# Performance work log

Hardware: AMD Instinct MI355X
Metric: run time of the kernel (lower is better)

## Reference

```python
import jax, jax.numpy as jnp
import numpy as np

DIM = 512
H = 8
HD = DIM // H  # head_dim = 64


def setup_inputs() -> dict:
    key = jax.random.key(0)
    k1, k2, k3 = jax.random.split(key, 3)
    B, N = 16, 4096
    x = jax.random.normal(k1, (B, DIM, N), jnp.float32)
    # qkv_proj: Conv1d(dim, H*(1+2*HD), kernel=1) == linear over channels
    Wqkv = jax.random.normal(k2, (H * (1 + 2 * HD), DIM), jnp.float32) * 0.02
    bqkv = jnp.zeros((H * (1 + 2 * HD),), jnp.float32)
    # proj: Conv1d(dim, dim, kernel=1)
    Wp = jax.random.normal(k3, (DIM, DIM), jnp.float32) * 0.02
    bp = jnp.zeros((DIM,), jnp.float32)
    return {"x": x, "Wqkv": Wqkv, "bqkv": bqkv, "Wp": Wp, "bp": bp}


def reference(x, Wqkv, bqkv, Wp, bp):
    B, C, N = x.shape
    # 1x1 conv projection -> [B, H*(1+2*HD), N]
    qkv = jnp.einsum('oc,bcn->bon', Wqkv, x) + bqkv[None, :, None]
    qkv = qkv.reshape(B, H, 1 + 2 * HD, N)
    q = qkv[:, :, 0:1, :]          # [B,H,1,N]
    k = qkv[:, :, 1:1 + HD, :]     # [B,H,HD,N]
    v = qkv[:, :, 1 + HD:, :]      # [B,H,HD,N]
    scores = jax.nn.softmax(q, axis=-1)              # softmax over N
    ctx = jnp.sum(k * scores, axis=-1, keepdims=True)  # [B,H,HD,1]
    out = jax.nn.relu(v) * ctx                         # [B,H,HD,N]
    # permute/split/cat in torch == [B,H,HD,N] -> [B,N,H*HD] -> [B,C,N]
    out = out.transpose(0, 3, 1, 2).reshape(B, N, H * HD)
    out = out.transpose(0, 2, 1)                       # [B,C,N]
    out = jnp.einsum('oc,bcn->bon', Wp, out) + bp[None, :, None]
    return out
```

## Files before the change

### kernel.cpp

```cpp
#include <hip/hip_runtime.h>

#define NB 16
#define NC 512
#define NN 4096
#define NH 8

typedef __attribute__((ext_vector_type(8))) __bf16 bf16x8;
typedef __attribute__((ext_vector_type(4))) float f32x4;

__device__ __forceinline__ unsigned short f2bf(float f) {
    union { float f; unsigned u; } x; x.f = f;
    unsigned r = x.u + 0x7FFF + ((x.u >> 16) & 1);
    return (unsigned short)(r >> 16);
}
__device__ __forceinline__ float bits2f(unsigned u) {
    union { unsigned u; float f; } x; x.u = u; return x.f;
}

__device__ __forceinline__ void async16(const void* g, const void* l) {
    __builtin_amdgcn_global_load_lds(
        (const __attribute__((address_space(1))) void*)g,
        (__attribute__((address_space(3))) void*)l, 16, 0, 0);
}

__global__ void pack_kernel(const float* __restrict__ Wqkv, const float* __restrict__ bqkv,
                            const float* __restrict__ Wp,
                            unsigned short* __restrict__ Wv_bf, unsigned short* __restrict__ Wp_bf,
                            float* __restrict__ bv) {
    int t = blockIdx.x * 256 + threadIdx.x;
    int j = t >> 9, c = t & 511;
    int h = j >> 6, d = j & 63;
    Wv_bf[t] = f2bf(Wqkv[((size_t)h * 129 + 65 + d) * 512 + c]);
    Wp_bf[t] = f2bf(Wp[t]);
    if (t < 512) bv[t] = bqkv[(t >> 6) * 129 + 65 + (t & 63)];
}

__global__ __launch_bounds__(256) void q_xbf_kernel(
        const float* __restrict__ x, const float* __restrict__ Wqkv,
        unsigned int* __restrict__ xbf, float* __restrict__ qP) {
    __shared__ float Ws[8][64];
    int n0 = blockIdx.x * 512, c0 = blockIdx.y * 64, b = blockIdx.z;
    int t = threadIdx.x;
    for (int i = t; i < 512; i += 256)
        Ws[i >> 6][i & 63] = Wqkv[(size_t)(i >> 6) * (129 * 512) + c0 + (i & 63)];
    __syncthreads();

    float acc[8][2];
#pragma unroll
    for (int h = 0; h < 8; h++) { acc[h][0] = 0.f; acc[h][1] = 0.f; }

    const float* xb = x + ((size_t)b * NC + c0) * NN + n0;
    unsigned int* ob = xbf + (((size_t)b * NC + c0) * NN + n0) / 2 + t;

#pragma unroll 4
    for (int c = 0; c < 64; c++) {
        float2 v = *((const float2*)(xb + (size_t)c * NN) + t);
        ob[(size_t)c * (NN / 2)] = (unsigned)f2bf(v.x) | ((unsigned)f2bf(v.y) << 16);
#pragma unroll
        for (int h = 0; h < 8; h++) {
            float w = Ws[h][c];
            acc[h][0] += w * v.x;
            acc[h][1] += w * v.y;
        }
    }
#pragma unroll
    for (int h = 0; h < 8; h++) {
        float2 o; o.x = acc[h][0]; o.y = acc[h][1];
        *((float2*)(qP + ((size_t)(blockIdx.y * NB + b) * 8 + h) * NN + n0) + t) = o;
    }
}

__global__ void softmax_kernel(const float* __restrict__ qP, float* __restrict__ sT) {
    int bh = blockIdx.x;
    int b = bh >> 3, h = bh & 7;
    int t = threadIdx.x;
    __shared__ float red[8];
    const float* qp = qP + (size_t)bh * NN;
    const size_t cstr = (size_t)NB * 8 * NN;
    float v[16];
    float mx = -1e30f;
#pragma unroll
    for (int i = 0; i < 16; i++) {
        int n = t + i * 256;
        float s = 0.f;
#pragma unroll
        for (int cb = 0; cb < 8; cb++) s += qp[cb * cstr + n];
        v[i] = s; mx = fmaxf(mx, s);
    }
#pragma unroll
    for (int o = 32; o; o >>= 1) mx = fmaxf(mx, __shfl_xor(mx, o));
    if ((t & 63) == 0) red[t >> 6] = mx;
    __syncthreads();
    mx = fmaxf(fmaxf(red[0], red[1]), fmaxf(red[2], red[3]));
    float s = 0.f;
#pragma unroll
    for (int i = 0; i < 16; i++) { v[i] = __expf(v[i] - mx); s += v[i]; }
#pragma unroll
    for (int o = 32; o; o >>= 1) s += __shfl_xor(s, o);
    __syncthreads();
    if ((t & 63) == 0) red[4 + (t >> 6)] = s;
    __syncthreads();
    float inv = 1.f / (red[4] + red[5] + red[6] + red[7]);
#pragma unroll
    for (int i = 0; i < 16; i++) {
        int n = t + i * 256;
        sT[((size_t)b * NN + n) * 8 + h] = v[i] * inv;
    }
}

__global__ __launch_bounds__(256) void xbar_kernel(
        const unsigned int* __restrict__ xbf, const float* __restrict__ sT,
        float* __restrict__ xbarP) {
    __shared__ float red[4][8][64];
    int c0 = blockIdx.x * 32, sl = blockIdx.y, b = blockIdx.z;
    int t = threadIdx.x;
    int l = t & 63, w = t >> 6;
    int nsl0 = sl * 512;
    float s_[8][8];
    {
        const f32x4* sp = (const f32x4*)(sT + ((size_t)b * NN + nsl0 + l * 8) * 8);
#pragma unroll
        for (int j = 0; j < 8; j++) {
            f32x4 a = sp[2 * j], bq = sp[2 * j + 1];
            s_[j][0] = a[0]; s_[j][1] = a[1]; s_[j][2] = a[2]; s_[j][3] = a[3];
            s_[j][4] = bq[0]; s_[j][5] = bq[1]; s_[j][6] = bq[2]; s_[j][7] = bq[3];
        }
    }
    float acc[8][8];
#pragma unroll
    for (int r = 0; r < 8; r++)
#pragma unroll
        for (int h = 0; h < 8; h++) acc[r][h] = 0.f;

    const unsigned int* xr = xbf + (((size_t)b * NC + c0 + w * 8) * NN + nsl0) / 2 + l * 4;
    uint4 xv = *(const uint4*)(xr);
#pragma unroll
    for (int r = 0; r < 8; r++) {
        uint4 cur = xv;
        if (r < 7) xv = *(const uint4*)(xr + (size_t)(r + 1) * (NN / 2));
        float xf[8];
        xf[0] = bits2f(cur.x << 16); xf[1] = bits2f(cur.x & 0xFFFF0000u);
        xf[2] = bits2f(cur.y << 16); xf[3] = bits2f(cur.y & 0xFFFF0000u);
        xf[4] = bits2f(cur.z << 16); xf[5] = bits2f(cur.z & 0xFFFF0000u);
        xf[6] = bits2f(cur.w << 16); xf[7] = bits2f(cur.w & 0xFFFF0000u);
#pragma unroll
        for (int j = 0; j < 8; j++)
#pragma unroll
            for (int h = 0; h < 8; h++) acc[r][h] += xf[j] * s_[j][h];
    }
#pragma unroll
    for (int r = 0; r < 8; r++)
#pragma unroll
        for (int h = 0; h < 8; h++) {
            float a = acc[r][h];
            a += __shfl_xor(a, 8);
            a += __shfl_xor(a, 16);
            a += __shfl_xor(a, 32);
            acc[r][h] = a;
        }
    if (l < 8) {
#pragma unroll
        for (int r = 0; r < 8; r++)
#pragma unroll
            for (int h = 0; h < 8; h++) red[w][l][r * 8 + h] = acc[r][h];
    }
    __syncthreads();
    {
        int idx = t & 63;
        float v = 0.f;
#pragma unroll
        for (int res = 0; res < 8; res++) v += red[w][res][idx];
        int r = idx >> 3, h = idx & 7;
        xbarP[(((size_t)sl * NB + b) * 8 + h) * NC + c0 + w * 8 + r] = v;
    }
}

__global__ void ctx_kernel(const float* __restrict__ xbarP, const float* __restrict__ Wqkv,
                           const float* __restrict__ bqkv, float* __restrict__ ctx) {
    int bh = blockIdx.x; int b = bh >> 3, h = bh & 7;
    int t = threadIdx.x;
    __shared__ float xb[512];
    for (int i = t; i < 512; i += 256) {
        float s = 0.f;
#pragma unroll
        for (int sl = 0; sl < 8; sl++) s += xbarP[(((size_t)sl * NB + b) * 8 + h) * NC + i];
        xb[i] = s;
    }
    __syncthreads();
    int d = t >> 2, sub = t & 3;
    const float* wk = Wqkv + ((size_t)h * 129 + 1 + d) * 512;
    float acc = 0.f;
    for (int i = sub * 4; i < 512; i += 16) {
        float4 w = *(const float4*)(wk + i);
        acc += w.x * xb[i] + w.y * xb[i + 1] + w.z * xb[i + 2] + w.w * xb[i + 3];
    }
    acc += __shfl_xor(acc, 1);
    acc += __shfl_xor(acc, 2);
    if (sub == 0) ctx[(size_t)b * NC + h * 64 + d] = acc + bqkv[h * 129 + 1 + d];
}

template <int MODE>
__global__ __launch_bounds__(512) void gemm_kernel(
    const unsigned short* __restrict__ A,
    const unsigned short* __restrict__ Bmat,
    const float* __restrict__ bias,
    const float* __restrict__ ctx,
    unsigned short* __restrict__ mT,
    float* __restrict__ outp)
{
    __shared__ alignas(16) unsigned short As[256 * 32];
    __shared__ alignas(16) unsigned short Bs[128 * 32];
    int b = blockIdx.z;
    int m0 = blockIdx.y * 256, n0 = blockIdx.x * 128;
    int t = threadIdx.x;
    int lane = t & 63;
    int wid = t >> 6;
    int wm = wid >> 1, wn = wid & 1;

    const unsigned short* Bb = Bmat + ((size_t)b * NN + n0) * NC;
    const unsigned int*   Bu = (const unsigned int*)Bmat + (size_t)b * NC * (NN / 2);

    int srow = lane >> 2, sc8 = (lane & 3) * 8;

    f32x4 acc[4][4];
#pragma unroll
    for (int i = 0; i < 4; i++)
#pragma unroll
        for (int j = 0; j < 4; j++) { f32x4 z = {0.f, 0.f, 0.f, 0.f}; acc[i][j] = z; }

    for (int kk = 0; kk < 512; kk += 32) {
        async16(A + (size_t)(m0 + wid * 32 + srow) * 512 + kk + sc8,      As + wid * 1024);
        async16(A + (size_t)(m0 + wid * 32 + 16 + srow) * 512 + kk + sc8, As + wid * 1024 + 512);
        if constexpr (MODE == 0) {
            int c = t >> 4, nb = (t & 15) * 8;
            uint4 xv = *(const uint4*)(Bu + ((size_t)(kk + c) * NN + n0 + nb) / 2);
            const unsigned short* xp16 = (const unsigned short*)&xv;
#pragma unroll
            for (int i = 0; i < 8; i++) {
                int nl = nb + i;
                int byte = nl * 64 + ((c * 2) ^ (((nl >> 3) & 3) << 4));
                *(unsigned short*)((char*)Bs + byte) = xp16[i];
            }
        } else {
            async16(Bb + (size_t)(wid * 16 + srow) * 512 + kk + sc8, Bs + wid * 512);
        }
        __syncthreads();
        bf16x8 af[4], bfr[4];
        int koff = (lane >> 4) * 8;
        int arow = wm * 64 + (lane & 15);
        int brow = wn * 64 + (lane & 15);
#pragma unroll
        for (int i = 0; i < 4; i++) af[i]  = *(const bf16x8*)(As + (size_t)(arow + i * 16) * 32 + koff);
#pragma unroll
        for (int j = 0; j < 4; j++) {
            if constexpr (MODE == 0) {
                int row = brow + j * 16;
                int byte = row * 64 + ((koff * 2) ^ (((row >> 3) & 3) << 4));
                bfr[j] = *(const bf16x8*)((const char*)Bs + byte);
            } else {
                bfr[j] = *(const bf16x8*)(Bs + (size_t)(brow + j * 16) * 32 + koff);
            }
        }
#pragma unroll
        for (int i = 0; i < 4; i++)
#pragma unroll
            for (int j = 0; j < 4; j++)
                acc[i][j] = __builtin_amdgcn_mfma_f32_16x16x32_bf16(af[i], bfr[j], acc[i][j], 0, 0, 0);
        __syncthreads();
    }

    int g = lane >> 4, col = lane & 15;
#pragma unroll
    for (int i = 0; i < 4; i++) {
        int j0 = m0 + wm * 64 + i * 16 + g * 4;
        if (MODE == 0) {
            float4 bv4 = *(const float4*)(bias + j0);
            float4 cx4 = *(const float4*)(ctx + (size_t)b * NC + j0);
#pragma unroll
            for (int j = 0; j < 4; j++) {
                int n = n0 + wn * 64 + j * 16 + col;
                f32x4 a = acc[i][j];
                unsigned short h0 = f2bf(fmaxf(a[0] + bv4.x, 0.f) * cx4.x);
                unsigned short h1 = f2bf(fmaxf(a[1] + bv4.y, 0.f) * cx4.y);
                unsigned short h2 = f2bf(fmaxf(a[2] + bv4.z, 0.f) * cx4.z);
                unsigned short h3 = f2bf(fmaxf(a[3] + bv4.w, 0.f) * cx4.w);
                uint2 pk;
                pk.x = (unsigned)h0 | ((unsigned)h1 << 16);
                pk.y = (unsigned)h2 | ((unsigned)h3 << 16);
                *(uint2*)(mT + ((size_t)b * NN + n) * NC + j0) = pk;
            }
        } else {
            float4 bp4 = *(const float4*)(bias + j0);
#pragma unroll
            for (int j = 0; j < 4; j++) {
                int n = n0 + wn * 64 + j * 16 + col;
                f32x4 a = acc[i][j];
                float* op = outp + (size_t)b * NC * NN + (size_t)j0 * NN + n;
                op[0]              = a[0] + bp4.x;
                op[NN]             = a[1] + bp4.y;
                op[2 * (size_t)NN] = a[2] + bp4.z;
                op[3 * (size_t)NN] = a[3] + bp4.w;
            }
        }
    }
}

extern "C" void kernel_launch(void* const* d_in, const int* in_sizes, int n_in,
                              void* d_out, int out_size, void* d_ws, size_t ws_size,
                              hipStream_t stream) {
    const float* x    = (const float*)d_in[0];
    const float* Wqkv = (const float*)d_in[1];
    const float* bqkv = (const float*)d_in[2];
    const float* Wp   = (const float*)d_in[3];
    const float* bp   = (const float*)d_in[4];
    float* outp = (float*)d_out;

    char* ws = (char*)d_ws;
    unsigned short* mT = (unsigned short*)ws;
    float* sT    = (float*)(ws + 2097152);
    float* qP    = (float*)(ws + 4194304);
    float* xbarP = (float*)(ws + 20971520);
    float* ctx   = (float*)(ws + 67108864);
    unsigned short* Wv_bf = (unsigned short*)(ws + 67108864 + 32768);
    unsigned short* Wp_bf = (unsigned short*)(ws + 67108864 + 32768 + 524288);
    float* bv    = (float*)(ws + 67108864 + 32768 + 1048576);
    unsigned int* xbf = (unsigned int*)d_out;

    pack_kernel<<<dim3(1024), 256, 0, stream>>>(Wqkv, bqkv, Wp, Wv_bf, Wp_bf, bv);
    q_xbf_kernel<<<dim3(8, 8, 16), 256, 0, stream>>>(x, Wqkv, xbf, qP);
    softmax_kernel<<<dim3(128), 256, 0, stream>>>(qP, sT);
    xbar_kernel<<<dim3(16, 8, 16), 256, 0, stream>>>(xbf, sT, xbarP);
    ctx_kernel<<<dim3(128), 256, 0, stream>>>(xbarP, Wqkv, bqkv, ctx);
    gemm_kernel<0><<<dim3(32, 2, 16), 512, 0, stream>>>(
        Wv_bf, (const unsigned short*)xbf, bv, ctx, mT, nullptr);
    gemm_kernel<1><<<dim3(32, 2, 16), 512, 0, stream>>>(
        Wp_bf, mT, bp, nullptr, nullptr, outp);
}
```

Before: 219.3 us.

## Fuse V-projection and output projection GEMMs, keeping intermediate in LDS

Merges the two GEMM kernels into one. Each block computes the full 512-channel V projection for a 128-column tile, applies relu and ctx scaling, stores the bf16 result in LDS, then runs the output projection from LDS. This removes the global round trip of the intermediate mT. The bf16 copy of x is dropped, so the q, xbar and fused kernels read fp32 x directly and convert on the fly. The cost is 144 KB of LDS per block, which limits occupancy, plus heavier register use and weights streamed straight from global memory into registers.

```diff
diff --git a/kernel.cpp b/kernel.cpp
--- a/kernel.cpp
+++ b/kernel.cpp
@@ -12,15 +12,6 @@
     union { float f; unsigned u; } x; x.f = f;
     unsigned r = x.u + 0x7FFF + ((x.u >> 16) & 1);
     return (unsigned short)(r >> 16);
-}
-__device__ __forceinline__ float bits2f(unsigned u) {
-    union { unsigned u; float f; } x; x.u = u; return x.f;
-}
-
-__device__ __forceinline__ void async16(const void* g, const void* l) {
-    __builtin_amdgcn_global_load_lds(
-        (const __attribute__((address_space(1))) void*)g,
-        (__attribute__((address_space(3))) void*)l, 16, 0, 0);
 }
 
 __global__ void pack_kernel(const float* __restrict__ Wqkv, const float* __restrict__ bqkv,
@@ -35,9 +26,9 @@
     if (t < 512) bv[t] = bqkv[(t >> 6) * 129 + 65 + (t & 63)];
 }
 
-__global__ __launch_bounds__(256) void q_xbf_kernel(
+__global__ __launch_bounds__(256) void q_kernel(
         const float* __restrict__ x, const float* __restrict__ Wqkv,
-        unsigned int* __restrict__ xbf, float* __restrict__ qP) {
+        float* __restrict__ qP) {
     __shared__ float Ws[8][64];
     int n0 = blockIdx.x * 512, c0 = blockIdx.y * 64, b = blockIdx.z;
     int t = threadIdx.x;
@@ -50,12 +41,9 @@
     for (int h = 0; h < 8; h++) { acc[h][0] = 0.f; acc[h][1] = 0.f; }
 
     const float* xb = x + ((size_t)b * NC + c0) * NN + n0;
-    unsigned int* ob = xbf + (((size_t)b * NC + c0) * NN + n0) / 2 + t;
-
 #pragma unroll 4
     for (int c = 0; c < 64; c++) {
         float2 v = *((const float2*)(xb + (size_t)c * NN) + t);
-        ob[(size_t)c * (NN / 2)] = (unsigned)f2bf(v.x) | ((unsigned)f2bf(v.y) << 16);
 #pragma unroll
         for (int h = 0; h < 8; h++) {
             float w = Ws[h][c];
@@ -109,7 +97,7 @@
 }
 
 __global__ __launch_bounds__(256) void xbar_kernel(
-        const unsigned int* __restrict__ xbf, const float* __restrict__ sT,
+        const float* __restrict__ x, const float* __restrict__ sT,
         float* __restrict__ xbarP) {
     __shared__ float red[4][8][64];
     int c0 = blockIdx.x * 32, sl = blockIdx.y, b = blockIdx.z;
@@ -132,17 +120,12 @@
 #pragma unroll
         for (int h = 0; h < 8; h++) acc[r][h] = 0.f;
 
-    const unsigned int* xr = xbf + (((size_t)b * NC + c0 + w * 8) * NN + nsl0) / 2 + l * 4;
-    uint4 xv = *(const uint4*)(xr);
+    const float* xr = x + ((size_t)b * NC + c0 + w * 8) * NN + nsl0 + l * 8;
 #pragma unroll
     for (int r = 0; r < 8; r++) {
-        uint4 cur = xv;
-        if (r < 7) xv = *(const uint4*)(xr + (size_t)(r + 1) * (NN / 2));
-        float xf[8];
-        xf[0] = bits2f(cur.x << 16); xf[1] = bits2f(cur.x & 0xFFFF0000u);
-        xf[2] = bits2f(cur.y << 16); xf[3] = bits2f(cur.y & 0xFFFF0000u);
-        xf[4] = bits2f(cur.z << 16); xf[5] = bits2f(cur.z & 0xFFFF0000u);
-        xf[6] = bits2f(cur.w << 16); xf[7] = bits2f(cur.w & 0xFFFF0000u);
+        float4 a0 = *(const float4*)(xr + (size_t)r * NN);
+        float4 a1 = *(const float4*)(xr + (size_t)r * NN + 4);
+        float xf[8] = {a0.x, a0.y, a0.z, a0.w, a1.x, a1.y, a1.z, a1.w};
 #pragma unroll
         for (int j = 0; j < 8; j++)
 #pragma unroll
@@ -199,108 +182,139 @@
     if (sub == 0) ctx[(size_t)b * NC + h * 64 + d] = acc + bqkv[h * 129 + 1 + d];
 }
 
-template <int MODE>
-__global__ __launch_bounds__(512) void gemm_kernel(
-    const unsigned short* __restrict__ A,
-    const unsigned short* __restrict__ Bmat,
-    const float* __restrict__ bias,
+__global__ __launch_bounds__(512, 2) void fused_gemm_kernel(
+    const unsigned short* __restrict__ Wv,
+    const unsigned short* __restrict__ Wp,
+    const float* __restrict__ x,
+    const float* __restrict__ bv,
+    const float* __restrict__ bp,
     const float* __restrict__ ctx,
-    unsigned short* __restrict__ mT,
     float* __restrict__ outp)
 {
-    __shared__ alignas(16) unsigned short As[256 * 32];
+    __shared__ alignas(16) unsigned short Ms[16 * 128 * 32];
     __shared__ alignas(16) unsigned short Bs[128 * 32];
-    int b = blockIdx.z;
-    int m0 = blockIdx.y * 256, n0 = blockIdx.x * 128;
-    int t = threadIdx.x;
-    int lane = t & 63;
-    int wid = t >> 6;
-    int wm = wid >> 1, wn = wid & 1;
-
-    const unsigned short* Bb = Bmat + ((size_t)b * NN + n0) * NC;
-    const unsigned int*   Bu = (const unsigned int*)Bmat + (size_t)b * NC * (NN / 2);
-
-    int srow = lane >> 2, sc8 = (lane & 3) * 8;
-
-    f32x4 acc[4][4];
-#pragma unroll
-    for (int i = 0; i < 4; i++)
+    int b = blockIdx.y, n0 = blockIdx.x * 128;
+    int t = threadIdx.x;
+    int lane = t & 63, wid = t >> 6;
+    int wj = wid >> 1, wn = wid & 1;
+    int g = lane >> 4, col = lane & 15;
+    int koff = g * 8;
+
+    int sc = t >> 4, sn8 = (t & 15) * 8;
+
+    f32x4 acc[8][4];
+#pragma unroll
+    for (int i = 0; i < 8; i++)
 #pragma unroll
         for (int j = 0; j < 4; j++) { f32x4 z = {0.f, 0.f, 0.f, 0.f}; acc[i][j] = z; }
 
-    for (int kk = 0; kk < 512; kk += 32) {
-        async16(A + (size_t)(m0 + wid * 32 + srow) * 512 + kk + sc8,      As + wid * 1024);
-        async16(A + (size_t)(m0 + wid * 32 + 16 + srow) * 512 + kk + sc8, As + wid * 1024 + 512);
-        if constexpr (MODE == 0) {
-            int c = t >> 4, nb = (t & 15) * 8;
-            uint4 xv = *(const uint4*)(Bu + ((size_t)(kk + c) * NN + n0 + nb) / 2);
-            const unsigned short* xp16 = (const unsigned short*)&xv;
+    bf16x8 afc[8], afn[8];
+#pragma unroll
+    for (int i = 0; i < 8; i++)
+        afc[i] = *(const bf16x8*)(Wv + (size_t)(wj * 128 + i * 16 + col) * 512 + koff);
+
+#pragma unroll 2
+    for (int ks = 0; ks < 16; ks++) {
+        int kk = ks * 32;
+        {
+            const float* xr = x + ((size_t)b * NC + kk + sc) * NN + n0 + sn8;
+            float4 v0 = *(const float4*)(xr);
+            float4 v1 = *(const float4*)(xr + 4);
+            unsigned short xv[8] = {f2bf(v0.x), f2bf(v0.y), f2bf(v0.z), f2bf(v0.w),
+                                    f2bf(v1.x), f2bf(v1.y), f2bf(v1.z), f2bf(v1.w)};
 #pragma unroll
             for (int i = 0; i < 8; i++) {
-                int nl = nb + i;
-                int byte = nl * 64 + ((c * 2) ^ (((nl >> 3) & 3) << 4));
-                *(unsigned short*)((char*)Bs + byte) = xp16[i];
+                int nl = sn8 + i;
+                int byte = nl * 64 + ((sc * 2) ^ (((nl >> 3) & 3) << 4));
+                *(unsigned short*)((char*)Bs + byte) = xv[i];
             }
-        } else {
-            async16(Bb + (size_t)(wid * 16 + srow) * 512 + kk + sc8, Bs + wid * 512);
+        }
+        if (ks < 15) {
+#pragma unroll
+            for (int i = 0; i < 8; i++)
+                afn[i] = *(const bf16x8*)(Wv + (size_t)(wj * 128 + i * 16 + col) * 512 + kk + 32 + koff);
         }
         __syncthreads();
-        bf16x8 af[4], bfr[4];
-        int koff = (lane >> 4) * 8;
-        int arow = wm * 64 + (lane & 15);
-        int brow = wn * 64 + (lane & 15);
-#pragma unroll
-        for (int i = 0; i < 4; i++) af[i]  = *(const bf16x8*)(As + (size_t)(arow + i * 16) * 32 + koff);
+        bf16x8 bfr[4];
 #pragma unroll
         for (int j = 0; j < 4; j++) {
-            if constexpr (MODE == 0) {
-                int row = brow + j * 16;
-                int byte = row * 64 + ((koff * 2) ^ (((row >> 3) & 3) << 4));
-                bfr[j] = *(const bf16x8*)((const char*)Bs + byte);
-            } else {
-                bfr[j] = *(const bf16x8*)(Bs + (size_t)(brow + j * 16) * 32 + koff);
-            }
-        }
-#pragma unroll
-        for (int i = 0; i < 4; i++)
+            int row = wn * 64 + j * 16 + col;
+            int byte = row * 64 + ((koff * 2) ^ (((row >> 3) & 3) << 4));
+            bfr[j] = *(const bf16x8*)((const char*)Bs + byte);
+        }
+#pragma unroll
+        for (int i = 0; i < 8; i++)
 #pragma unroll
             for (int j = 0; j < 4; j++)
-                acc[i][j] = __builtin_amdgcn_mfma_f32_16x16x32_bf16(af[i], bfr[j], acc[i][j], 0, 0, 0);
+                acc[i][j] = __builtin_amdgcn_mfma_f32_16x16x32_bf16(afc[i], bfr[j], acc[i][j], 0, 0, 0);
         __syncthreads();
-    }
-
-    int g = lane >> 4, col = lane & 15;
-#pragma unroll
-    for (int i = 0; i < 4; i++) {
-        int j0 = m0 + wm * 64 + i * 16 + g * 4;
-        if (MODE == 0) {
-            float4 bv4 = *(const float4*)(bias + j0);
-            float4 cx4 = *(const float4*)(ctx + (size_t)b * NC + j0);
-#pragma unroll
-            for (int j = 0; j < 4; j++) {
-                int n = n0 + wn * 64 + j * 16 + col;
-                f32x4 a = acc[i][j];
-                unsigned short h0 = f2bf(fmaxf(a[0] + bv4.x, 0.f) * cx4.x);
-                unsigned short h1 = f2bf(fmaxf(a[1] + bv4.y, 0.f) * cx4.y);
-                unsigned short h2 = f2bf(fmaxf(a[2] + bv4.z, 0.f) * cx4.z);
-                unsigned short h3 = f2bf(fmaxf(a[3] + bv4.w, 0.f) * cx4.w);
-                uint2 pk;
-                pk.x = (unsigned)h0 | ((unsigned)h1 << 16);
-                pk.y = (unsigned)h2 | ((unsigned)h3 << 16);
-                *(uint2*)(mT + ((size_t)b * NN + n) * NC + j0) = pk;
-            }
-        } else {
-            float4 bp4 = *(const float4*)(bias + j0);
-#pragma unroll
-            for (int j = 0; j < 4; j++) {
-                int n = n0 + wn * 64 + j * 16 + col;
-                f32x4 a = acc[i][j];
-                float* op = outp + (size_t)b * NC * NN + (size_t)j0 * NN + n;
-                op[0]              = a[0] + bp4.x;
-                op[NN]             = a[1] + bp4.y;
-                op[2 * (size_t)NN] = a[2] + bp4.z;
-                op[3 * (size_t)NN] = a[3] + bp4.w;
-            }
+#pragma unroll
+        for (int i = 0; i < 8; i++) afc[i] = afn[i];
+    }
+
+#pragma unroll
+    for (int i = 0; i < 8; i++) {
+        int j0 = wj * 128 + i * 16 + g * 4;
+        float4 bv4 = *(const float4*)(bv + j0);
+        float4 cx4 = *(const float4*)(ctx + (size_t)b * NC + j0);
+#pragma unroll
+        for (int j = 0; j < 4; j++) {
+            int n = wn * 64 + j * 16 + col;
+            f32x4 a = acc[i][j];
+            unsigned short h0 = f2bf(fmaxf(a[0] + bv4.x, 0.f) * cx4.x);
+            unsigned short h1 = f2bf(fmaxf(a[1] + bv4.y, 0.f) * cx4.y);
+            unsigned short h2 = f2bf(fmaxf(a[2] + bv4.z, 0.f) * cx4.z);
+            unsigned short h3 = f2bf(fmaxf(a[3] + bv4.w, 0.f) * cx4.w);
+            uint2 pk;
+            pk.x = (unsigned)h0 | ((unsigned)h1 << 16);
+            pk.y = (unsigned)h2 | ((unsigned)h3 << 16);
+            *(uint2*)(Ms + (size_t)(j0 >> 5) * 4096 + n * 32 + (j0 & 31)) = pk;
+        }
+    }
+    __syncthreads();
+
+#pragma unroll
+    for (int i = 0; i < 8; i++)
+#pragma unroll
+        for (int j = 0; j < 4; j++) { f32x4 z = {0.f, 0.f, 0.f, 0.f}; acc[i][j] = z; }
+#pragma unroll
+    for (int i = 0; i < 8; i++)
+        afc[i] = *(const bf16x8*)(Wp + (size_t)(wj * 128 + i * 16 + col) * 512 + koff);
+
+#pragma unroll 2
+    for (int ks = 0; ks < 16; ks++) {
+        int kk = ks * 32;
+        if (ks < 15) {
+#pragma unroll
+            for (int i = 0; i < 8; i++)
+                afn[i] = *(const bf16x8*)(Wp + (size_t)(wj * 128 + i * 16 + col) * 512 + kk + 32 + koff);
+        }
+        bf16x8 bfr[4];
+#pragma unroll
+        for (int j = 0; j < 4; j++)
+            bfr[j] = *(const bf16x8*)(Ms + (size_t)ks * 4096 + (wn * 64 + j * 16 + col) * 32 + koff);
+#pragma unroll
+        for (int i = 0; i < 8; i++)
+#pragma unroll
+            for (int j = 0; j < 4; j++)
+                acc[i][j] = __builtin_amdgcn_mfma_f32_16x16x32_bf16(afc[i], bfr[j], acc[i][j], 0, 0, 0);
+#pragma unroll
+        for (int i = 0; i < 8; i++) afc[i] = afn[i];
+    }
+
+#pragma unroll
+    for (int i = 0; i < 8; i++) {
+        int o0 = wj * 128 + i * 16 + g * 4;
+        float4 bp4 = *(const float4*)(bp + o0);
+#pragma unroll
+        for (int j = 0; j < 4; j++) {
+            int n = n0 + wn * 64 + j * 16 + col;
+            f32x4 a = acc[i][j];
+            float* op = outp + ((size_t)b * NC + o0) * NN + n;
+            op[0]              = a[0] + bp4.x;
+            op[NN]             = a[1] + bp4.y;
+            op[2 * (size_t)NN] = a[2] + bp4.z;
+            op[3 * (size_t)NN] = a[3] + bp4.w;
         }
     }
 }
@@ -316,23 +330,18 @@
     float* outp = (float*)d_out;
 
     char* ws = (char*)d_ws;
-    unsigned short* mT = (unsigned short*)ws;
-    float* sT    = (float*)(ws + 2097152);
-    float* qP    = (float*)(ws + 4194304);
-    float* xbarP = (float*)(ws + 20971520);
-    float* ctx   = (float*)(ws + 67108864);
-    unsigned short* Wv_bf = (unsigned short*)(ws + 67108864 + 32768);
-    unsigned short* Wp_bf = (unsigned short*)(ws + 67108864 + 32768 + 524288);
-    float* bv    = (float*)(ws + 67108864 + 32768 + 1048576);
-    unsigned int* xbf = (unsigned int*)d_out;
+    float* sT    = (float*)(ws);
+    float* qP    = (float*)(ws + 2097152);
+    float* xbarP = (float*)(ws + 18874368);
+    float* ctx   = (float*)(ws + 20971520);
+    unsigned short* Wv_bf = (unsigned short*)(ws + 20971520 + 32768);
+    unsigned short* Wp_bf = (unsigned short*)(ws + 20971520 + 32768 + 524288);
+    float* bv    = (float*)(ws + 20971520 + 32768 + 1048576);
 
     pack_kernel<<<dim3(1024), 256, 0, stream>>>(Wqkv, bqkv, Wp, Wv_bf, Wp_bf, bv);
-    q_xbf_kernel<<<dim3(8, 8, 16), 256, 0, stream>>>(x, Wqkv, xbf, qP);
+    q_kernel<<<dim3(8, 8, 16), 256, 0, stream>>>(x, Wqkv, qP);
     softmax_kernel<<<dim3(128), 256, 0, stream>>>(qP, sT);
-    xbar_kernel<<<dim3(16, 8, 16), 256, 0, stream>>>(xbf, sT, xbarP);
+    xbar_kernel<<<dim3(16, 8, 16), 256, 0, stream>>>(x, sT, xbarP);
     ctx_kernel<<<dim3(128), 256, 0, stream>>>(xbarP, Wqkv, bqkv, ctx);
-    gemm_kernel<0><<<dim3(32, 2, 16), 512, 0, stream>>>(
-        Wv_bf, (const unsigned short*)xbf, bv, ctx, mT, nullptr);
-    gemm_kernel<1><<<dim3(32, 2, 16), 512, 0, stream>>>(
-        Wp_bf, mT, bp, nullptr, nullptr, outp);
-}
+    fused_gemm_kernel<<<dim3(32, 16), 512, 0, stream>>>(Wv_bf, Wp_bf, x, bv, bp, ctx, outp);
+}
```

Measured after the change: 231.0 us. +5.3%, slower.
